# Optimization experiments

Hardware: AMD Instinct MI355X
Metric: run time of the kernel (lower is better)

The kernel has to match this reference:

```python
import jax, jax.numpy as jnp
import numpy as np

N_NODES = 100000
N_GRAPHS = 64
EPS = 1e-5


def _sage_conv(x, src, dst, Wl, bl, Wr):
    # mean-aggregate neighbor messages (src -> dst), then lin_l(agg) + lin_r(x)
    n = x.shape[0]
    deg = jax.ops.segment_sum(jnp.ones_like(dst, dtype=x.dtype), dst, num_segments=n)
    agg = jax.ops.segment_sum(x[src], dst, num_segments=n)  # [N, d]
    agg = agg / jnp.maximum(deg, 1.0)[:, None]
    return agg @ Wl + bl + x @ Wr


def _bn_relu(x, gamma, beta):
    mu = jnp.mean(x, axis=0)
    var = jnp.var(x, axis=0)
    return jax.nn.relu((x - mu) * jax.lax.rsqrt(var + EPS) * gamma + beta)


def setup_inputs() -> dict:
    key = jax.random.key(0)
    ks = jax.random.split(key, 16)
    E = 1600000
    x = jax.random.normal(ks[0], (N_NODES, 2), dtype=jnp.float32)
    edge_index = jax.random.randint(ks[1], (2, E), 0, N_NODES, dtype=jnp.int64)
    batch = jnp.sort(jax.random.randint(ks[2], (N_NODES,), 0, N_GRAPHS, dtype=jnp.int64))

    def lin(k, din, dout):
        s = 1.0 / np.sqrt(din)
        return jax.random.uniform(k, (din, dout), jnp.float32, -s, s)

    d = {"x": x, "edge_index": edge_index, "batch": batch}
    dims = [(2, 32), (32, 64), (64, 128)]
    for i, (din, dout) in enumerate(dims, 1):
        k1, k2 = jax.random.split(ks[2 + i])
        d[f"Wl{i}"] = lin(k1, din, dout)
        d[f"bl{i}"] = jnp.zeros((dout,), jnp.float32)
        d[f"Wr{i}"] = lin(k2, din, dout)
        d[f"g{i}"] = jnp.ones((dout,), jnp.float32)
        d[f"be{i}"] = jnp.zeros((dout,), jnp.float32)
    d["Wf1"] = lin(ks[10], 128, 64)
    d["bf1"] = jnp.zeros((64,), jnp.float32)
    d["Wf2"] = lin(ks[11], 64, 1)
    d["bf2"] = jnp.zeros((1,), jnp.float32)
    return d


def reference(x, edge_index, batch,
              Wl1, bl1, Wr1, g1, be1,
              Wl2, bl2, Wr2, g2, be2,
              Wl3, bl3, Wr3, g3, be3,
              Wf1, bf1, Wf2, bf2):
    src, dst = edge_index[0], edge_index[1]
    h = _bn_relu(_sage_conv(x, src, dst, Wl1, bl1, Wr1), g1, be1)
    h = _bn_relu(_sage_conv(h, src, dst, Wl2, bl2, Wr2), g2, be2)
    h = _bn_relu(_sage_conv(h, src, dst, Wl3, bl3, Wr3), g3, be3)
    # global mean pool over graphs
    cnt = jax.ops.segment_sum(jnp.ones_like(batch, dtype=h.dtype), batch, num_segments=N_GRAPHS)
    pooled = jax.ops.segment_sum(h, batch, num_segments=N_GRAPHS) / jnp.maximum(cnt, 1.0)[:, None]
    out = jax.nn.relu(pooled @ Wf1 + bf1)
    # dropout is identity in eval mode
    return out @ Wf2 + bf2
```

## Files before the change

### kernel.cpp

```cpp
#include <hip/hip_runtime.h>
#include <hip/hip_fp16.h>

#define N_NODES 100000
#define N_GRAPHS 64
#define BN_EPS 1e-5

#define NB 782
#define NC 49
#define PT1 4096
#define PT2 2048
#define BPC 16
#define CAP 3072

__device__ __forceinline__ float bfly64(float v) {
#pragma unroll
    for (int m = 1; m < 64; m <<= 1) v += __shfl_xor(v, m, 64);
    return v;
}

__device__ __forceinline__ unsigned pack_h2(float a, float b) {
    __half2 h = __floats2half2_rn(a, b);
    unsigned w;
    __builtin_memcpy(&w, &h, 4);
    return w;
}

__device__ __forceinline__ float2 unpack_h2(unsigned w) {
    __half2 h;
    __builtin_memcpy(&h, &w, 4);
    return __half22float2(h);
}

__global__ void hist_fine(const int* __restrict__ dst, int* __restrict__ bhist, int E) {
    __shared__ int h[NB];
    for (int i = threadIdx.x; i < NB; i += 256) h[i] = 0;
    __syncthreads();
    int stride = gridDim.x * 256;
    for (int e = blockIdx.x * 256 + threadIdx.x; e < E; e += stride) {
        int d = __builtin_nontemporal_load(dst + e);
        atomicAdd(&h[d >> 7], 1);
    }
    __syncthreads();
    for (int i = threadIdx.x; i < NB; i += 256)
        if (h[i]) atomicAdd(&bhist[i], h[i]);
}

__global__ void scan_buckets(const int* __restrict__ bhist, int* __restrict__ bo,
                             int* __restrict__ fcur, int* __restrict__ co,
                             int* __restrict__ ccur) {
    __shared__ int sh[1024];
    int t = threadIdx.x;
    sh[t] = (t < NB) ? bhist[t] : 0;
    __syncthreads();
    for (int st = 1; st < 1024; st <<= 1) {
        int v = (t >= st) ? sh[t - st] : 0;
        __syncthreads();
        sh[t] += v;
        __syncthreads();
    }
    int total = sh[NB - 1];
    if (t < NB) {
        int e = t ? sh[t - 1] : 0;
        bo[t] = e; fcur[t] = e;
    } else if (t < 784) {
        if (t == NB) bo[NB] = total;
        fcur[t] = total;
    }
    if (t < NC) {
        int i = t << 4;
        int e = i ? sh[i - 1] : 0;
        co[t] = e; ccur[t] = e;
    } else if (t == NC) {
        co[NC] = total;
    }
}

__global__ __launch_bounds__(256)
void part1(const int* __restrict__ dst, const int* __restrict__ src,
           int* __restrict__ ccur, int* __restrict__ cdst, int* __restrict__ csrc, int E) {
    __shared__ int ld[PT1], ls[PT1];
    __shared__ unsigned char lb[PT1];
    __shared__ int hist[NC], lbase[NC], gbase[NC];
    long long t0 = (long long)blockIdx.x * PT1;
    int n = (int)min((long long)PT1, (long long)E - t0);
    int tid = threadIdx.x;
    for (int i = tid; i < NC; i += 256) hist[i] = 0;
    __syncthreads();
    int d[PT1 / 256], s[PT1 / 256], c[PT1 / 256];
#pragma unroll
    for (int k = 0; k < PT1 / 256; ++k) {
        int li = k * 256 + tid;
        if (li < n) {
            d[k] = __builtin_nontemporal_load(dst + t0 + li);
            s[k] = __builtin_nontemporal_load(src + t0 + li);
            c[k] = d[k] >> 11;
            atomicAdd(&hist[c[k]], 1);
        }
    }
    __syncthreads();
    if (tid == 0) {
        int run = 0;
        for (int i = 0; i < NC; ++i) { lbase[i] = run; run += hist[i]; }
    }
    __syncthreads();
    if (tid < NC) gbase[tid] = atomicAdd(&ccur[tid], hist[tid]);
    __syncthreads();
    for (int i = tid; i < NC; i += 256) hist[i] = 0;
    __syncthreads();
#pragma unroll
    for (int k = 0; k < PT1 / 256; ++k) {
        int li = k * 256 + tid;
        if (li < n) {
            int pos = lbase[c[k]] + atomicAdd(&hist[c[k]], 1);
            ld[pos] = d[k]; ls[pos] = s[k]; lb[pos] = (unsigned char)c[k];
        }
    }
    __syncthreads();
    for (int i = tid; i < n; i += 256) {
        int bb = lb[i];
        int g = gbase[bb] + (i - lbase[bb]);
        cdst[g] = ld[i];
        csrc[g] = ls[i];
    }
}

__global__ __launch_bounds__(256)
void part2(const int* __restrict__ cdst, const int* __restrict__ csrc,
           const int* __restrict__ co, int* __restrict__ fcur,
           int* __restrict__ qdst, int* __restrict__ qsrc) {
    __shared__ int ld[PT2], ls[PT2];
    __shared__ unsigned char lb[PT2];
    __shared__ int hist[16], lbase[16], gbase[16];
    int c = blockIdx.x / BPC;
    int j = blockIdx.x % BPC;
    int beg = co[c], end = co[c + 1];
    int tid = threadIdx.x;
    for (int t0 = beg + j * PT2; t0 < end; t0 += BPC * PT2) {
        int n = min(PT2, end - t0);
        if (tid < 16) hist[tid] = 0;
        __syncthreads();
        int d[PT2 / 256], s[PT2 / 256], f[PT2 / 256];
#pragma unroll
        for (int k = 0; k < PT2 / 256; ++k) {
            int li = k * 256 + tid;
            if (li < n) {
                d[k] = cdst[t0 + li];
                s[k] = csrc[t0 + li];
                f[k] = (d[k] >> 7) & 15;
                atomicAdd(&hist[f[k]], 1);
            }
        }
        __syncthreads();
        if (tid == 0) {
            int run = 0;
            for (int i = 0; i < 16; ++i) { lbase[i] = run; run += hist[i]; }
        }
        __syncthreads();
        if (tid < 16) gbase[tid] = atomicAdd(&fcur[(c << 4) + tid], hist[tid]);
        __syncthreads();
        if (tid < 16) hist[tid] = 0;
        __syncthreads();
#pragma unroll
        for (int k = 0; k < PT2 / 256; ++k) {
            int li = k * 256 + tid;
            if (li < n) {
                int pos = lbase[f[k]] + atomicAdd(&hist[f[k]], 1);
                ld[pos] = d[k]; ls[pos] = s[k]; lb[pos] = (unsigned char)f[k];
            }
        }
        __syncthreads();
        for (int i = tid; i < n; i += 256) {
            int bb = lb[i];
            int g = gbase[bb] + (i - lbase[bb]);
            qdst[g] = ld[i];
            qsrc[g] = ls[i];
        }
        __syncthreads();
    }
}

__global__ __launch_bounds__(256)
void fill_final(const int* __restrict__ qdst, const int* __restrict__ qsrc,
                const int* __restrict__ bo, int* __restrict__ offs,
                int* __restrict__ nbr, int N, int E) {
    __shared__ int cnt[128], cbase[128], cur[128];
    __shared__ int lout[CAP];
    int b = blockIdx.x;
    int nlo = b << 7;
    int nn = min(128, N - nlo);
    int ebeg = bo[b], ne = bo[b + 1] - ebeg;
    int tid = threadIdx.x;
    if (tid < 128) { cnt[tid] = 0; cur[tid] = 0; }
    __syncthreads();
    for (int i = tid; i < ne; i += 256)
        atomicAdd(&cnt[qdst[ebeg + i] - nlo], 1);
    __syncthreads();
    if (tid < 128) cbase[tid] = cnt[tid];
    __syncthreads();
    for (int st = 1; st < 128; st <<= 1) {
        int v = 0;
        if (tid < 128 && tid >= st) v = cbase[tid - st];
        __syncthreads();
        if (tid < 128 && tid >= st) cbase[tid] += v;
        __syncthreads();
    }
    if (tid < nn)
        offs[nlo + tid] = ebeg + (tid ? cbase[tid - 1] : 0);
    if (b == NB - 1 && tid == 0) offs[N] = E;
    __syncthreads();
    for (int i = tid; i < ne; i += 256) {
        int d = qdst[ebeg + i];
        int s = qsrc[ebeg + i];
        int ln = d - nlo;
        int p = (ln ? cbase[ln - 1] : 0) + atomicAdd(&cur[ln], 1);
        lout[p] = s;
    }
    __syncthreads();
    for (int i = tid; i < ne; i += 256)
        nbr[ebeg + i] = lout[i];
}

__global__ __launch_bounds__(256)
void layer1_fused(const float2* __restrict__ x2,
                  const int* __restrict__ offs, const int* __restrict__ nbr,
                  const float* __restrict__ Wl, const float* __restrict__ bl,
                  const float* __restrict__ Wr,
                  __half* __restrict__ hout16,
                  double* __restrict__ sums, int N) {
    __shared__ float sAr[64];
    int tid = threadIdx.x;
    if (tid < 64) sAr[tid] = 0.f;
    __syncthreads();
    int n = blockIdx.x * 256 + tid;
    bool valid = (n < N);
    int beg = 0, end = 0;
    if (valid) { beg = offs[n]; end = offs[n + 1]; }
    double ax = 0.0, ay = 0.0;
    int j = beg;
    for (; j + 4 <= end; j += 4) {
        int s0 = nbr[j], s1 = nbr[j + 1], s2 = nbr[j + 2], s3 = nbr[j + 3];
        float2 v0 = x2[s0], v1 = x2[s1], v2 = x2[s2], v3 = x2[s3];
        ax += v0.x; ay += v0.y;
        ax += v1.x; ay += v1.y;
        ax += v2.x; ay += v2.y;
        ax += v3.x; ay += v3.y;
    }
    for (; j < end; ++j) {
        float2 v = x2[nbr[j]];
        ax += v.x; ay += v.y;
    }
    float invd = 1.0f / fmaxf((float)(end - beg), 1.0f);
    float a0 = (float)ax * invd, a1 = (float)ay * invd;
    float x0 = 0.f, x1 = 0.f;
    if (valid) {
        float2 xv = x2[n];
        x0 = xv.x; x1 = xv.y;
    }
    float acc[32];
#pragma unroll
    for (int jj = 0; jj < 32; ++jj)
        acc[jj] = bl[jj] + a0 * Wl[jj] + a1 * Wl[32 + jj] + x0 * Wr[jj] + x1 * Wr[32 + jj];
    if (valid) {
        unsigned w[16];
#pragma unroll
        for (int p = 0; p < 16; ++p) w[p] = pack_h2(acc[2*p], acc[2*p+1]);
        uint4* q = (uint4*)(hout16 + (size_t)n * 32);
        q[0] = make_uint4(w[0], w[1], w[2], w[3]);
        q[1] = make_uint4(w[4], w[5], w[6], w[7]);
        q[2] = make_uint4(w[8], w[9], w[10], w[11]);
        q[3] = make_uint4(w[12], w[13], w[14], w[15]);
    }
    int lane = tid & 63;
#pragma unroll
    for (int jj = 0; jj < 32; ++jj) {
        float v = valid ? acc[jj] : 0.f;
        float s = bfly64(v);
        float q = bfly64(v * v);
        if (lane == jj) atomicAdd(&sAr[jj], s);
        if (lane == 32 + jj) atomicAdd(&sAr[32 + jj], q);
    }
    __syncthreads();
    if (tid < 64) atomicAdd(&sums[tid], (double)sAr[tid]);
}

template<int F>
__global__ __launch_bounds__(256)
void agg_h16(const uint2* __restrict__ xh, const int* __restrict__ offs,
             const int* __restrict__ nbr,
             const double* __restrict__ sums,
             const float* __restrict__ gamma, const float* __restrict__ beta,
             uint2* __restrict__ aggh, int N) {
    constexpr int FV = F / 4;
    constexpr int NPB = 256 / FV;
    __shared__ float lsc[F], lsf[F];
    int tid = threadIdx.y * FV + threadIdx.x;
    if (tid < F) {
        double mu = sums[tid] / (double)N_NODES;
        double var = sums[F + tid] / (double)N_NODES - mu * mu;
        if (var < 0.0) var = 0.0;
        double sc = (double)gamma[tid] / sqrt(var + BN_EPS);
        lsc[tid] = (float)sc;
        lsf[tid] = (float)((double)beta[tid] - mu * sc);
    }
    __syncthreads();
    int n = blockIdx.x * NPB + threadIdx.y;
    if (n >= N) return;
    int f = threadIdx.x;
    float4 sc = ((const float4*)lsc)[f];
    float4 sf = ((const float4*)lsf)[f];
    int beg = offs[n], end = offs[n + 1];
    double ax = 0.0, ay = 0.0, az = 0.0, aw = 0.0;
    int j = beg;
    for (; j + 8 <= end; j += 8) {
        int s[8];
#pragma unroll
        for (int u = 0; u < 8; ++u) s[u] = __builtin_nontemporal_load(nbr + j + u);
        uint2 uv[8];
#pragma unroll
        for (int u = 0; u < 8; ++u) uv[u] = xh[(long long)s[u] * FV + f];
#pragma unroll
        for (int u = 0; u < 8; ++u) {
            float2 f0 = unpack_h2(uv[u].x);
            float2 f1 = unpack_h2(uv[u].y);
            ax += fmaxf(f0.x * sc.x + sf.x, 0.f);
            ay += fmaxf(f0.y * sc.y + sf.y, 0.f);
            az += fmaxf(f1.x * sc.z + sf.z, 0.f);
            aw += fmaxf(f1.y * sc.w + sf.w, 0.f);
        }
    }
    for (; j + 4 <= end; j += 4) {
        int s[4];
#pragma unroll
        for (int u = 0; u < 4; ++u) s[u] = __builtin_nontemporal_load(nbr + j + u);
        uint2 uv[4];
#pragma unroll
        for (int u = 0; u < 4; ++u) uv[u] = xh[(long long)s[u] * FV + f];
#pragma unroll
        for (int u = 0; u < 4; ++u) {
            float2 f0 = unpack_h2(uv[u].x);
            float2 f1 = unpack_h2(uv[u].y);
            ax += fmaxf(f0.x * sc.x + sf.x, 0.f);
            ay += fmaxf(f0.y * sc.y + sf.y, 0.f);
            az += fmaxf(f1.x * sc.z + sf.z, 0.f);
            aw += fmaxf(f1.y * sc.w + sf.w, 0.f);
        }
    }
    for (; j < end; ++j) {
        int s = __builtin_nontemporal_load(nbr + j);
        uint2 uv = xh[(long long)s * FV + f];
        float2 f0 = unpack_h2(uv.x);
        float2 f1 = unpack_h2(uv.y);
        ax += fmaxf(f0.x * sc.x + sf.x, 0.f);
        ay += fmaxf(f0.y * sc.y + sf.y, 0.f);
        az += fmaxf(f1.x * sc.z + sf.z, 0.f);
        aw += fmaxf(f1.y * sc.w + sf.w, 0.f);
    }
    uint2 out;
    out.x = pack_h2((float)ax, (float)ay);
    out.y = pack_h2((float)az, (float)aw);
    aggh[(long long)n * FV + f] = out;
}

template<int DIN, int DOUT, int TN>
__global__ __launch_bounds__(256)
void linear_t2(const __half* __restrict__ xin16, const __half* __restrict__ agg16,
               const int* __restrict__ offs,
               const float* __restrict__ Wl, const float* __restrict__ bl,
               const float* __restrict__ Wr,
               const double* __restrict__ sumsIn,
               const float* __restrict__ gIn, const float* __restrict__ beIn,
               __half* __restrict__ hout16, int N) {
    constexpr int JT = 32;
    constexpr int NG = DOUT / JT;
    static_assert(TN * NG == 256, "cfg");
    constexpr int STRIDE = DIN + 1;
    constexpr int DIV4 = DIN / 4;
    constexpr int NV4 = TN * DIN / 4;
    __shared__ float shT[TN * STRIDE];
    __shared__ float shD[TN];
    __shared__ float lscIn[DIN], lsfIn[DIN];

    int tid = threadIdx.x;
    if (tid < DIN) {
        double mu = sumsIn[tid] / (double)N_NODES;
        double var = sumsIn[DIN + tid] / (double)N_NODES - mu * mu;
        if (var < 0.0) var = 0.0;
        double sc = (double)gIn[tid] / sqrt(var + BN_EPS);
        lscIn[tid] = (float)sc;
        lsfIn[tid] = (float)((double)beIn[tid] - mu * sc);
    }

    int n0 = blockIdx.x * TN;
    const uint2* __restrict__ gA = (const uint2*)(agg16 + (size_t)n0 * DIN);
#pragma unroll
    for (int it = 0; it < NV4 / 256; ++it) {
        int i = it * 256 + tid;
        int row = i / DIV4, col = (i % DIV4) * 4;
        uint2 uv = gA[i];
        float2 f0 = unpack_h2(uv.x);
        float2 f1 = unpack_h2(uv.y);
        float* p = &shT[row * STRIDE + col];
        p[0] = f0.x; p[1] = f0.y; p[2] = f1.x; p[3] = f1.y;
    }
    for (int i = tid; i < TN; i += 256) {
        int nn = min(n0 + i, N - 1);
        shD[i] = 1.0f / fmaxf((float)(offs[nn + 1] - offs[nn]), 1.0f);
    }
    __syncthreads();

    int tn = tid % TN;
    int jg = __builtin_amdgcn_readfirstlane(tid / TN);
    float invd = shD[tn];
    float acc[JT];
#pragma unroll
    for (int j = 0; j < JT; ++j) acc[j] = bl[jg * JT + j];

#pragma unroll 4
    for (int k = 0; k < DIN; ++k) {
        float a = shT[tn * STRIDE + k] * invd;
        const float* __restrict__ wlp = Wl + (size_t)k * DOUT + jg * JT;
#pragma unroll
        for (int j = 0; j < JT; ++j) acc[j] += a * wlp[j];
    }
    __syncthreads();

    const uint2* __restrict__ gX = (const uint2*)(xin16 + (size_t)n0 * DIN);
#pragma unroll
    for (int it = 0; it < NV4 / 256; ++it) {
        int i = it * 256 + tid;
        int row = i / DIV4, col4 = i % DIV4;
        uint2 uv = gX[i];
        float2 f0 = unpack_h2(uv.x);
        float2 f1 = unpack_h2(uv.y);
        float4 sc = ((const float4*)lscIn)[col4];
        float4 sf = ((const float4*)lsfIn)[col4];
        float* q = &shT[row * STRIDE + col4 * 4];
        q[0] = fmaxf(f0.x * sc.x + sf.x, 0.f);
        q[1] = fmaxf(f0.y * sc.y + sf.y, 0.f);
        q[2] = fmaxf(f1.x * sc.z + sf.z, 0.f);
        q[3] = fmaxf(f1.y * sc.w + sf.w, 0.f);
    }
    __syncthreads();

#pragma unroll 4
    for (int k = 0; k < DIN; ++k) {
        float xv = shT[tn * STRIDE + k];
        const float* __restrict__ wrp = Wr + (size_t)k * DOUT + jg * JT;
#pragma unroll
        for (int j = 0; j < JT; ++j) acc[j] += xv * wrp[j];
    }

    if (n0 + tn < N) {
        unsigned w[16];
#pragma unroll
        for (int p = 0; p < 16; ++p) w[p] = pack_h2(acc[2*p], acc[2*p+1]);
        uint4* qh = (uint4*)(hout16 + (size_t)(n0 + tn) * DOUT + jg * JT);
        qh[0] = make_uint4(w[0], w[1], w[2], w[3]);
        qh[1] = make_uint4(w[4], w[5], w[6], w[7]);
        qh[2] = make_uint4(w[8], w[9], w[10], w[11]);
        qh[3] = make_uint4(w[12], w[13], w[14], w[15]);
    }
}

template<int F>
__global__ __launch_bounds__(256)
void stats_partial(const uint4* __restrict__ h, float* __restrict__ partial, int N) {
    constexpr int P4 = F / 8;
    constexpr int R = 256 / P4;
    constexpr int NV = P4 * 16;
    __shared__ float lds[4 * NV];
    int tid = threadIdx.x;
    int p = tid % P4;
    int r = tid / P4;
    float s[8], q[8];
#pragma unroll
    for (int j = 0; j < 8; ++j) { s[j] = 0.f; q[j] = 0.f; }
    for (int n = blockIdx.x * R + r; n < N; n += 1024 * R) {
        uint4 v = h[(size_t)n * P4 + p];
        float2 a = unpack_h2(v.x), b = unpack_h2(v.y), c = unpack_h2(v.z), d = unpack_h2(v.w);
        s[0] += a.x; q[0] += a.x * a.x;
        s[1] += a.y; q[1] += a.y * a.y;
        s[2] += b.x; q[2] += b.x * b.x;
        s[3] += b.y; q[3] += b.y * b.y;
        s[4] += c.x; q[4] += c.x * c.x;
        s[5] += c.y; q[5] += c.y * c.y;
        s[6] += d.x; q[6] += d.x * d.x;
        s[7] += d.y; q[7] += d.y * d.y;
    }
    for (int m = P4; m < 64; m <<= 1) {
#pragma unroll
        for (int j = 0; j < 8; ++j) {
            s[j] += __shfl_xor(s[j], m, 64);
            q[j] += __shfl_xor(q[j], m, 64);
        }
    }
    int wave = tid >> 6;
    int lane = tid & 63;
    if (lane < P4) {
#pragma unroll
        for (int j = 0; j < 8; ++j) {
            lds[wave * NV + lane * 16 + j] = s[j];
            lds[wave * NV + lane * 16 + 8 + j] = q[j];
        }
    }
    __syncthreads();
    for (int v = tid; v < NV; v += 256) {
        float t0 = lds[v] + lds[NV + v] + lds[2 * NV + v] + lds[3 * NV + v];
        int pp = v >> 4, k = v & 15;
        int feat = pp * 8 + (k & 7);
        int out = (k < 8) ? feat : (F + feat);
        partial[(size_t)blockIdx.x * (2 * F) + out] = t0;
    }
}

template<int F>
__global__ __launch_bounds__(256)
void stats_finalize(const float* __restrict__ partial, double* __restrict__ sums) {
    __shared__ double sh[256];
    int i = blockIdx.x;
    int t = threadIdx.x;
    double a = 0.0;
#pragma unroll
    for (int k = 0; k < 4; ++k)
        a += (double)partial[(size_t)(t + k * 256) * (2 * F) + i];
    sh[t] = a;
    __syncthreads();
    for (int st = 128; st > 0; st >>= 1) {
        if (t < st) sh[t] += sh[t + st];
        __syncthreads();
    }
    if (t == 0) sums[i] = sh[0];
}

__global__ void pool_partial(const __half* __restrict__ h, const int* __restrict__ batch,
                             const double* __restrict__ sums,
                             const float* __restrict__ gamma, const float* __restrict__ beta,
                             double* __restrict__ pooled_d, int N) {
    __shared__ float lsc[128], lsf[128];
    const int CH = 64;
    int f = threadIdx.x;
    {
        double mu = sums[f] / (double)N_NODES;
        double var = sums[128 + f] / (double)N_NODES - mu * mu;
        if (var < 0.0) var = 0.0;
        double sc = (double)gamma[f] / sqrt(var + BN_EPS);
        lsc[f] = (float)sc;
        lsf[f] = (float)((double)beta[f] - mu * sc);
    }
    __syncthreads();
    int n0 = blockIdx.x * CH;
    if (n0 >= N) return;
    int n1 = min(n0 + CH, N);
    float sc = lsc[f], sf = lsf[f];
    int g = batch[n0];
    float acc = 0.f;
    for (int n = n0; n < n1; ++n) {
        int bg = batch[n];
        if (bg != g) {
            atomicAdd(&pooled_d[g * 128 + f], (double)acc);
            acc = 0.f;
            g = bg;
        }
        float v = __half2float(h[(long long)n * 128 + f]);
        acc += fmaxf(v * sc + sf, 0.f);
    }
    atomicAdd(&pooled_d[g * 128 + f], (double)acc);
}

__global__ void mlp_fused(const double* __restrict__ pooled_d, const int* __restrict__ batch,
                          const float* __restrict__ Wf1, const float* __restrict__ bf1,
                          const float* __restrict__ Wf2, const float* __restrict__ bf2,
                          float* __restrict__ out, int N) {
    __shared__ float sp[128];
    int g = blockIdx.x;
    int t = threadIdx.x;
    int lo = 0, hi = N;
    while (lo < hi) { int m = (lo + hi) >> 1; if (batch[m] < g) lo = m + 1; else hi = m; }
    int start = lo;
    hi = N;
    while (lo < hi) { int m = (lo + hi) >> 1; if (batch[m] < g + 1) lo = m + 1; else hi = m; }
    int cnt = lo - start;
    sp[t] = (float)(pooled_d[g * 128 + t] / (double)max(cnt, 1));
    __syncthreads();
    if (t < 64) {
        float hacc = bf1[t];
#pragma unroll 8
        for (int k = 0; k < 128; ++k) hacc += sp[k] * Wf1[k * 64 + t];
        hacc = fmaxf(hacc, 0.f) * Wf2[t];
        for (int o = 32; o > 0; o >>= 1) hacc += __shfl_down(hacc, o);
        if (t == 0) out[g] = hacc + bf2[0];
    }
}

extern "C" void kernel_launch(void* const* d_in, const int* in_sizes, int n_in,
                              void* d_out, int out_size, void* d_ws, size_t ws_size,
                              hipStream_t stream) {
    const float* x     = (const float*)d_in[0];
    const int*   ei    = (const int*)d_in[1];
    const int*   batch = (const int*)d_in[2];
    const float *Wl1=(const float*)d_in[3],  *bl1=(const float*)d_in[4],  *Wr1=(const float*)d_in[5];
    const float *g1 =(const float*)d_in[6],  *be1=(const float*)d_in[7];
    const float *Wl2=(const float*)d_in[8],  *bl2=(const float*)d_in[9],  *Wr2=(const float*)d_in[10];
    const float *g2 =(const float*)d_in[11], *be2=(const float*)d_in[12];
    const float *Wl3=(const float*)d_in[13], *bl3=(const float*)d_in[14], *Wr3=(const float*)d_in[15];
    const float *g3 =(const float*)d_in[16], *be3=(const float*)d_in[17];
    const float *Wf1=(const float*)d_in[18], *bf1=(const float*)d_in[19];
    const float *Wf2=(const float*)d_in[20], *bf2=(const float*)d_in[21];

    const int N = N_NODES;
    const int E = in_sizes[1] / 2;
    const int* src = ei;
    const int* dst = ei + E;

    char* ws = (char*)d_ws;
    size_t off = 0;
    auto salloc = [&](size_t bytes) {
        void* p = ws + off;
        off += (bytes + 255) & ~(size_t)255;
        return p;
    };
    int*    bhist   = (int*)   salloc(NB * 4);
    double* sums    = (double*)salloc(768 * 8);
    double* pooledd = (double*)salloc((size_t)N_GRAPHS * 128 * 8);
    size_t zero_bytes = off;
    int*    offs    = (int*)   salloc((size_t)(N + 1) * 4);
    int*    bo      = (int*)   salloc((NB + 1) * 4);
    int*    fcur    = (int*)   salloc(784 * 4);
    int*    co      = (int*)   salloc((NC + 1) * 4);
    int*    ccur    = (int*)   salloc(NC * 4);
    int*    nbr     = (int*)   salloc((size_t)E * 4);
    float*  partial = (float*) salloc((size_t)1024 * 256 * 4);
    __half* h1h     = (__half*)salloc((size_t)(N + 256) * 32 * 2);
    __half* h2h     = (__half*)salloc((size_t)(N + 256) * 64 * 2);
    __half* h3h     = (__half*)salloc((size_t)(N + 256) * 128 * 2);
    __half* aggh    = (__half*)salloc((size_t)(N + 256) * 64 * 2);
    (void)ws_size;

    double* sums1 = sums, *sums2 = sums + 256, *sums3 = sums + 512;
    int* cdst = (int*)h3h;
    int* csrc = cdst + E;
    int* qdst = (int*)aggh;
    int* qsrc = qdst + E;

    hipMemsetAsync(bhist, 0, zero_bytes, stream);

    hist_fine<<<1024, 256, 0, stream>>>(dst, bhist, E);
    scan_buckets<<<1, 1024, 0, stream>>>(bhist, bo, fcur, co, ccur);
    part1<<<(E + PT1 - 1) / PT1, 256, 0, stream>>>(dst, src, ccur, cdst, csrc, E);
    part2<<<NC * BPC, 256, 0, stream>>>(cdst, csrc, co, fcur, qdst, qsrc);
    fill_final<<<NB, 256, 0, stream>>>(qdst, qsrc, bo, offs, nbr, N, E);

    const int NL = (N + 255) / 256;

    layer1_fused<<<NL, 256, 0, stream>>>((const float2*)x, offs, nbr,
                                          Wl1, bl1, Wr1, h1h, sums1, N);

    agg_h16<32><<<(N + 31) / 32, dim3(8, 32), 0, stream>>>(
        (const uint2*)h1h, offs, nbr, sums1, g1, be1, (uint2*)aggh, N);
    linear_t2<32, 64, 128><<<(N + 127) / 128, 256, 0, stream>>>(
        h1h, aggh, offs, Wl2, bl2, Wr2, sums1, g1, be1, h2h, N);
    stats_partial<64><<<1024, 256, 0, stream>>>((const uint4*)h2h, partial, N);
    stats_finalize<64><<<128, 256, 0, stream>>>(partial, sums2);

    agg_h16<64><<<(N + 15) / 16, dim3(16, 16), 0, stream>>>(
        (const uint2*)h2h, offs, nbr, sums2, g2, be2, (uint2*)aggh, N);
    linear_t2<64, 128, 64><<<(N + 63) / 64, 256, 0, stream>>>(
        h2h, aggh, offs, Wl3, bl3, Wr3, sums2, g2, be2, h3h, N);
    stats_partial<128><<<1024, 256, 0, stream>>>((const uint4*)h3h, partial, N);
    stats_finalize<128><<<256, 256, 0, stream>>>(partial, sums3);

    pool_partial<<<(N + 63) / 64, 128, 0, stream>>>(h3h, batch, sums3, g3, be3, pooledd, N);
    mlp_fused<<<N_GRAPHS, 128, 0, stream>>>(pooledd, batch, Wf1, bf1, Wf2, bf2, (float*)d_out, N);
}
```

Measured before the change: 377.1 us.

## Use MFMA fp16 hi/lo split for SAGE linears and fuse BN stats

Replaces the scalar fp32 linear kernels for layers 2 and 3 with MFMA 16x16x32 f16 matrix ops. Weights are prepacked into fp16 high and low parts so the product keeps near-fp32 weight precision. Per-block column sums and squared sums are computed in the epilogue, removing the separate stats_partial pass that re-read the outputs. In exchange, activations are rounded to fp16 before the matmul, output stores become narrower, and a small weight-packing kernel is added.

```diff
diff --git a/kernel.cpp b/kernel.cpp
--- a/kernel.cpp
+++ b/kernel.cpp
@@ -11,6 +11,15 @@
 #define PT2 2048
 #define BPC 16
 #define CAP 3072
+
+typedef _Float16 f16x8 __attribute__((ext_vector_type(8)));
+typedef float f32x4 __attribute__((ext_vector_type(4)));
+
+union F16x8u {
+    f16x8 v;
+    __half2 h2[4];
+    uint4 u;
+};
 
 __device__ __forceinline__ float bfly64(float v) {
 #pragma unroll
@@ -361,168 +370,177 @@
     aggh[(long long)n * FV + f] = out;
 }
 
-template<int DIN, int DOUT, int TN>
 __global__ __launch_bounds__(256)
-void linear_t2(const __half* __restrict__ xin16, const __half* __restrict__ agg16,
-               const int* __restrict__ offs,
-               const float* __restrict__ Wl, const float* __restrict__ bl,
-               const float* __restrict__ Wr,
-               const double* __restrict__ sumsIn,
-               const float* __restrict__ gIn, const float* __restrict__ beIn,
-               __half* __restrict__ hout16, int N) {
-    constexpr int JT = 32;
-    constexpr int NG = DOUT / JT;
-    static_assert(TN * NG == 256, "cfg");
-    constexpr int STRIDE = DIN + 1;
-    constexpr int DIV4 = DIN / 4;
-    constexpr int NV4 = TN * DIN / 4;
-    __shared__ float shT[TN * STRIDE];
-    __shared__ float shD[TN];
-    __shared__ float lscIn[DIN], lsfIn[DIN];
-
+void pack_w(const float* __restrict__ Wl2, const float* __restrict__ Wr2,
+            const float* __restrict__ Wl3, const float* __restrict__ Wr3,
+            __half* __restrict__ pk) {
+    int e = blockIdx.x * 256 + threadIdx.x;
+    const float* W; int le, DOUT, NCB, base, SZ;
+    if (e < 2048)       { W = Wl2; le = e;         DOUT = 64;  NCB = 4; base = 0;     SZ = 2048; }
+    else if (e < 4096)  { W = Wr2; le = e - 2048;  DOUT = 64;  NCB = 4; base = 4096;  SZ = 2048; }
+    else if (e < 12288) { W = Wl3; le = e - 4096;  DOUT = 128; NCB = 8; base = 8192;  SZ = 8192; }
+    else                { W = Wr3; le = e - 12288; DOUT = 128; NCB = 8; base = 24576; SZ = 8192; }
+    int i = le & 7;
+    int lane = (le >> 3) & 63;
+    int cbkb = le >> 9;
+    int cb = cbkb % NCB;
+    int kb = cbkb / NCB;
+    int k = kb * 32 + ((lane >> 4) << 3) + i;
+    int col = cb * 16 + (lane & 15);
+    float w = W[k * DOUT + col];
+    __half h = __float2half(w);
+    float lo = w - __half2float(h);
+    pk[base + le] = h;
+    pk[base + SZ + le] = __float2half(lo);
+}
+
+template<int DIN, int DOUT>
+__global__ __launch_bounds__(256)
+void linear_mfma(const __half* __restrict__ xin16, const __half* __restrict__ agg16,
+                 const int* __restrict__ offs,
+                 const __half* __restrict__ wlhi, const __half* __restrict__ wllo,
+                 const __half* __restrict__ wrhi, const __half* __restrict__ wrlo,
+                 const float* __restrict__ bl,
+                 const double* __restrict__ sumsIn,
+                 const float* __restrict__ gIn, const float* __restrict__ beIn,
+                 __half* __restrict__ hout16, float* __restrict__ partial, int N) {
+    constexpr int KB = DIN / 32;
+    constexpr int NCB = DOUT / 16;
+    constexpr int MREP = 2;
+    constexpr int MB = 4 * MREP * 16;
+    __shared__ float lsc[DIN], lsf[DIN];
+    __shared__ float shInvd[MB];
+    __shared__ float blkS[DOUT], blkQ[DOUT];
     int tid = threadIdx.x;
     if (tid < DIN) {
         double mu = sumsIn[tid] / (double)N_NODES;
         double var = sumsIn[DIN + tid] / (double)N_NODES - mu * mu;
         if (var < 0.0) var = 0.0;
         double sc = (double)gIn[tid] / sqrt(var + BN_EPS);
-        lscIn[tid] = (float)sc;
-        lsfIn[tid] = (float)((double)beIn[tid] - mu * sc);
-    }
-
-    int n0 = blockIdx.x * TN;
-    const uint2* __restrict__ gA = (const uint2*)(agg16 + (size_t)n0 * DIN);
-#pragma unroll
-    for (int it = 0; it < NV4 / 256; ++it) {
-        int i = it * 256 + tid;
-        int row = i / DIV4, col = (i % DIV4) * 4;
-        uint2 uv = gA[i];
-        float2 f0 = unpack_h2(uv.x);
-        float2 f1 = unpack_h2(uv.y);
-        float* p = &shT[row * STRIDE + col];
-        p[0] = f0.x; p[1] = f0.y; p[2] = f1.x; p[3] = f1.y;
-    }
-    for (int i = tid; i < TN; i += 256) {
+        lsc[tid] = (float)sc;
+        lsf[tid] = (float)((double)beIn[tid] - mu * sc);
+    }
+    for (int i = tid; i < DOUT; i += 256) { blkS[i] = 0.f; blkQ[i] = 0.f; }
+    int n0 = blockIdx.x * MB;
+    for (int i = tid; i < MB; i += 256) {
         int nn = min(n0 + i, N - 1);
-        shD[i] = 1.0f / fmaxf((float)(offs[nn + 1] - offs[nn]), 1.0f);
-    }
-    __syncthreads();
-
-    int tn = tid % TN;
-    int jg = __builtin_amdgcn_readfirstlane(tid / TN);
-    float invd = shD[tn];
-    float acc[JT];
-#pragma unroll
-    for (int j = 0; j < JT; ++j) acc[j] = bl[jg * JT + j];
-
-#pragma unroll 4
-    for (int k = 0; k < DIN; ++k) {
-        float a = shT[tn * STRIDE + k] * invd;
-        const float* __restrict__ wlp = Wl + (size_t)k * DOUT + jg * JT;
-#pragma unroll
-        for (int j = 0; j < JT; ++j) acc[j] += a * wlp[j];
-    }
-    __syncthreads();
-
-    const uint2* __restrict__ gX = (const uint2*)(xin16 + (size_t)n0 * DIN);
-#pragma unroll
-    for (int it = 0; it < NV4 / 256; ++it) {
-        int i = it * 256 + tid;
-        int row = i / DIV4, col4 = i % DIV4;
-        uint2 uv = gX[i];
-        float2 f0 = unpack_h2(uv.x);
-        float2 f1 = unpack_h2(uv.y);
-        float4 sc = ((const float4*)lscIn)[col4];
-        float4 sf = ((const float4*)lsfIn)[col4];
-        float* q = &shT[row * STRIDE + col4 * 4];
-        q[0] = fmaxf(f0.x * sc.x + sf.x, 0.f);
-        q[1] = fmaxf(f0.y * sc.y + sf.y, 0.f);
-        q[2] = fmaxf(f1.x * sc.z + sf.z, 0.f);
-        q[3] = fmaxf(f1.y * sc.w + sf.w, 0.f);
-    }
-    __syncthreads();
-
-#pragma unroll 4
-    for (int k = 0; k < DIN; ++k) {
-        float xv = shT[tn * STRIDE + k];
-        const float* __restrict__ wrp = Wr + (size_t)k * DOUT + jg * JT;
-#pragma unroll
-        for (int j = 0; j < JT; ++j) acc[j] += xv * wrp[j];
-    }
-
-    if (n0 + tn < N) {
-        unsigned w[16];
-#pragma unroll
-        for (int p = 0; p < 16; ++p) w[p] = pack_h2(acc[2*p], acc[2*p+1]);
-        uint4* qh = (uint4*)(hout16 + (size_t)(n0 + tn) * DOUT + jg * JT);
-        qh[0] = make_uint4(w[0], w[1], w[2], w[3]);
-        qh[1] = make_uint4(w[4], w[5], w[6], w[7]);
-        qh[2] = make_uint4(w[8], w[9], w[10], w[11]);
-        qh[3] = make_uint4(w[12], w[13], w[14], w[15]);
+        shInvd[i] = 1.0f / fmaxf((float)(offs[nn + 1] - offs[nn]), 1.0f);
+    }
+    __syncthreads();
+
+    int wave = tid >> 6;
+    int lane = tid & 63;
+    int rlane = lane & 15;
+    int kg = lane >> 4;
+    int rbase = n0 + wave * (MREP * 16);
+
+    f16x8 aA[MREP][KB], aX[MREP][KB];
+#pragma unroll
+    for (int m = 0; m < MREP; ++m) {
+        int row = rbase + m * 16 + rlane;
+        int rowc = min(row, N - 1);
+        float invd = shInvd[wave * (MREP * 16) + m * 16 + rlane];
+#pragma unroll
+        for (int kb = 0; kb < KB; ++kb) {
+            int c0 = kb * 32 + kg * 8;
+            F16x8u ta, tx;
+            ta.u = *(const uint4*)(agg16 + (size_t)rowc * DIN + c0);
+            tx.u = *(const uint4*)(xin16 + (size_t)rowc * DIN + c0);
+#pragma unroll
+            for (int q = 0; q < 4; ++q) {
+                float2 fa = __half22float2(ta.h2[q]);
+                ta.h2[q] = __floats2half2_rn(fa.x * invd, fa.y * invd);
+                float2 fx = __half22float2(tx.h2[q]);
+                int c = c0 + 2 * q;
+                fx.x = fmaxf(fx.x * lsc[c] + lsf[c], 0.f);
+                fx.y = fmaxf(fx.y * lsc[c + 1] + lsf[c + 1], 0.f);
+                tx.h2[q] = __floats2half2_rn(fx.x, fx.y);
+            }
+            aA[m][kb] = ta.v;
+            aX[m][kb] = tx.v;
+        }
+    }
+
+    f32x4 acc[MREP][NCB];
+#pragma unroll
+    for (int cb = 0; cb < NCB; ++cb) {
+        float bv = bl[cb * 16 + rlane];
+#pragma unroll
+        for (int m = 0; m < MREP; ++m)
+            acc[m][cb] = {bv, bv, bv, bv};
+    }
+
+#pragma unroll
+    for (int cb = 0; cb < NCB; ++cb) {
+#pragma unroll
+        for (int kb = 0; kb < KB; ++kb) {
+            size_t fo = ((size_t)(kb * NCB + cb) * 64 + lane) * 8;
+            f16x8 blh = *(const f16x8*)(wlhi + fo);
+            f16x8 bll = *(const f16x8*)(wllo + fo);
+            f16x8 brh = *(const f16x8*)(wrhi + fo);
+            f16x8 brl = *(const f16x8*)(wrlo + fo);
+#pragma unroll
+            for (int m = 0; m < MREP; ++m) {
+                acc[m][cb] = __builtin_amdgcn_mfma_f32_16x16x32_f16(aA[m][kb], blh, acc[m][cb], 0, 0, 0);
+                acc[m][cb] = __builtin_amdgcn_mfma_f32_16x16x32_f16(aA[m][kb], bll, acc[m][cb], 0, 0, 0);
+                acc[m][cb] = __builtin_amdgcn_mfma_f32_16x16x32_f16(aX[m][kb], brh, acc[m][cb], 0, 0, 0);
+                acc[m][cb] = __builtin_amdgcn_mfma_f32_16x16x32_f16(aX[m][kb], brl, acc[m][cb], 0, 0, 0);
+            }
+        }
+    }
+
+#pragma unroll
+    for (int m = 0; m < MREP; ++m) {
+        int rowb = rbase + m * 16 + kg * 4;
+#pragma unroll
+        for (int r = 0; r < 4; ++r) {
+            int node = rowb + r;
+            if (node < N) {
+#pragma unroll
+                for (int cb = 0; cb < NCB; ++cb)
+                    hout16[(size_t)node * DOUT + cb * 16 + rlane] = __float2half(acc[m][cb][r]);
+            }
+        }
+    }
+
+#pragma unroll
+    for (int cb = 0; cb < NCB; ++cb) {
+        float s = 0.f, q = 0.f;
+#pragma unroll
+        for (int m = 0; m < MREP; ++m) {
+            int rowb = rbase + m * 16 + kg * 4;
+#pragma unroll
+            for (int r = 0; r < 4; ++r) {
+                if (rowb + r < N) {
+                    float v = acc[m][cb][r];
+                    s += v; q += v * v;
+                }
+            }
+        }
+        s += __shfl_xor(s, 16, 64); s += __shfl_xor(s, 32, 64);
+        q += __shfl_xor(q, 16, 64); q += __shfl_xor(q, 32, 64);
+        if (kg == 0) {
+            atomicAdd(&blkS[cb * 16 + rlane], s);
+            atomicAdd(&blkQ[cb * 16 + rlane], q);
+        }
+    }
+    __syncthreads();
+    float* po = partial + (size_t)blockIdx.x * (2 * DOUT);
+    for (int i = tid; i < DOUT; i += 256) {
+        po[i] = blkS[i];
+        po[DOUT + i] = blkQ[i];
     }
 }
 
 template<int F>
 __global__ __launch_bounds__(256)
-void stats_partial(const uint4* __restrict__ h, float* __restrict__ partial, int N) {
-    constexpr int P4 = F / 8;
-    constexpr int R = 256 / P4;
-    constexpr int NV = P4 * 16;
-    __shared__ float lds[4 * NV];
-    int tid = threadIdx.x;
-    int p = tid % P4;
-    int r = tid / P4;
-    float s[8], q[8];
-#pragma unroll
-    for (int j = 0; j < 8; ++j) { s[j] = 0.f; q[j] = 0.f; }
-    for (int n = blockIdx.x * R + r; n < N; n += 1024 * R) {
-        uint4 v = h[(size_t)n * P4 + p];
-        float2 a = unpack_h2(v.x), b = unpack_h2(v.y), c = unpack_h2(v.z), d = unpack_h2(v.w);
-        s[0] += a.x; q[0] += a.x * a.x;
-        s[1] += a.y; q[1] += a.y * a.y;
-        s[2] += b.x; q[2] += b.x * b.x;
-        s[3] += b.y; q[3] += b.y * b.y;
-        s[4] += c.x; q[4] += c.x * c.x;
-        s[5] += c.y; q[5] += c.y * c.y;
-        s[6] += d.x; q[6] += d.x * d.x;
-        s[7] += d.y; q[7] += d.y * d.y;
-    }
-    for (int m = P4; m < 64; m <<= 1) {
-#pragma unroll
-        for (int j = 0; j < 8; ++j) {
-            s[j] += __shfl_xor(s[j], m, 64);
-            q[j] += __shfl_xor(q[j], m, 64);
-        }
-    }
-    int wave = tid >> 6;
-    int lane = tid & 63;
-    if (lane < P4) {
-#pragma unroll
-        for (int j = 0; j < 8; ++j) {
-            lds[wave * NV + lane * 16 + j] = s[j];
-            lds[wave * NV + lane * 16 + 8 + j] = q[j];
-        }
-    }
-    __syncthreads();
-    for (int v = tid; v < NV; v += 256) {
-        float t0 = lds[v] + lds[NV + v] + lds[2 * NV + v] + lds[3 * NV + v];
-        int pp = v >> 4, k = v & 15;
-        int feat = pp * 8 + (k & 7);
-        int out = (k < 8) ? feat : (F + feat);
-        partial[(size_t)blockIdx.x * (2 * F) + out] = t0;
-    }
-}
-
-template<int F>
-__global__ __launch_bounds__(256)
-void stats_finalize(const float* __restrict__ partial, double* __restrict__ sums) {
+void stats_finalize2(const float* __restrict__ partial, double* __restrict__ sums, int P) {
     __shared__ double sh[256];
     int i = blockIdx.x;
     int t = threadIdx.x;
     double a = 0.0;
-#pragma unroll
-    for (int k = 0; k < 4; ++k)
-        a += (double)partial[(size_t)(t + k * 256) * (2 * F) + i];
+    for (int k = t; k < P; k += 256)
+        a += (double)partial[(size_t)k * (2 * F) + i];
     sh[t] = a;
     __syncthreads();
     for (int st = 128; st > 0; st >>= 1) {
@@ -630,6 +648,7 @@
     int*    ccur    = (int*)   salloc(NC * 4);
     int*    nbr     = (int*)   salloc((size_t)E * 4);
     float*  partial = (float*) salloc((size_t)1024 * 256 * 4);
+    __half* pk      = (__half*)salloc((size_t)40960 * 2);
     __half* h1h     = (__half*)salloc((size_t)(N + 256) * 32 * 2);
     __half* h2h     = (__half*)salloc((size_t)(N + 256) * 64 * 2);
     __half* h3h     = (__half*)salloc((size_t)(N + 256) * 128 * 2);
@@ -642,7 +661,14 @@
     int* qdst = (int*)aggh;
     int* qsrc = qdst + E;
 
+    const __half *pwl2h = pk,         *pwl2l = pk + 2048;
+    const __half *pwr2h = pk + 4096,  *pwr2l = pk + 6144;
+    const __half *pwl3h = pk + 8192,  *pwl3l = pk + 16384;
+    const __half *pwr3h = pk + 24576, *pwr3l = pk + 32768;
+
     hipMemsetAsync(bhist, 0, zero_bytes, stream);
+
+    pack_w<<<80, 256, 0, stream>>>(Wl2, Wr2, Wl3, Wr3, pk);
 
     hist_fine<<<1024, 256, 0, stream>>>(dst, bhist, E);
     scan_buckets<<<1, 1024, 0, stream>>>(bhist, bo, fcur, co, ccur);
@@ -651,23 +677,24 @@
     fill_final<<<NB, 256, 0, stream>>>(qdst, qsrc, bo, offs, nbr, N, E);
 
     const int NL = (N + 255) / 256;
+    const int NBLK = (N + 127) / 128;
 
     layer1_fused<<<NL, 256, 0, stream>>>((const float2*)x, offs, nbr,
                                           Wl1, bl1, Wr1, h1h, sums1, N);
 
     agg_h16<32><<<(N + 31) / 32, dim3(8, 32), 0, stream>>>(
         (const uint2*)h1h, offs, nbr, sums1, g1, be1, (uint2*)aggh, N);
-    linear_t2<32, 64, 128><<<(N + 127) / 128, 256, 0, stream>>>(
-        h1h, aggh, offs, Wl2, bl2, Wr2, sums1, g1, be1, h2h, N);
-    stats_partial<64><<<1024, 256, 0, stream>>>((const uint4*)h2h, partial, N);
-    stats_finalize<64><<<128, 256, 0, stream>>>(partial, sums2);
+    linear_mfma<32, 64><<<NBLK, 256, 0, stream>>>(
+        h1h, aggh, offs, pwl2h, pwl2l, pwr2h, pwr2l, bl2,
+        sums1, g1, be1, h2h, partial, N);
+    stats_finalize2<64><<<128, 256, 0, stream>>>(partial, sums2, NBLK);
 
     agg_h16<64><<<(N + 15) / 16, dim3(16, 16), 0, stream>>>(
         (const uint2*)h2h, offs, nbr, sums2, g2, be2, (uint2*)aggh, N);
-    linear_t2<64, 128, 64><<<(N + 63) / 64, 256, 0, stream>>>(
-        h2h, aggh, offs, Wl3, bl3, Wr3, sums2, g2, be2, h3h, N);
-    stats_partial<128><<<1024, 256, 0, stream>>>((const uint4*)h3h, partial, N);
-    stats_finalize<128><<<256, 256, 0, stream>>>(partial, sums3);
+    linear_mfma<64, 128><<<NBLK, 256, 0, stream>>>(
+        h2h, aggh, offs, pwl3h, pwl3l, pwr3h, pwr3l, bl3,
+        sums2, g2, be2, h3h, partial, N);
+    stats_finalize2<128><<<256, 256, 0, stream>>>(partial, sums3, NBLK);
 
     pool_partial<<<(N + 63) / 64, 128, 0, stream>>>(h3h, batch, sums3, g3, be3, pooledd, N);
     mlp_fused<<<N_GRAPHS, 128, 0, stream>>>(pooledd, batch, Wf1, bf1, Wf2, bf2, (float*)d_out, N);
```

New measurement: 346.5 us. -8.1%, faster.
